# Performance work log

Measured on AMD Instinct MI355X. Metric: run time of the kernel, lower is better.

## Reference

```python
import jax, jax.numpy as jnp
import numpy as np

BS, NA = 32, 128
NE = NA * (NA - 1)            # fully-connected directed, no self loops
NU, D = 4, 8                  # num_user, per-user feature dim
FEAT = NU * D                 # 32: node / edge feature dim
CC = 8                        # conv1 out channels (1x1 conv, in_channels=2)
CONV_OUT = CC * NU * D        # 256
EMB = 64                      # embedding size (x_last / output dim)
H1 = 256                      # MLP hidden
MLP1_IN = CONV_OUT + EMB      # layer_idx > 1: concat local_state_j
MLP2_IN = FEAT + EMB + EMB    # x0, x_last, agg_in


def make_edges():
    src, dst = np.meshgrid(np.arange(NA), np.arange(NA), indexing='ij')
    m = src != dst
    return jnp.asarray(np.stack([src[m], dst[m]], axis=1), dtype=jnp.int32)


def setup_inputs() -> dict:
    key = jax.random.key(0)
    ks = jax.random.split(key, 9)
    return {
        "x0": jax.random.normal(ks[0], (BS, NA, FEAT), jnp.float32),
        "x_last": jax.random.normal(ks[1], (BS, NA, EMB), jnp.float32),
        "edge_attr": jax.random.normal(ks[2], (BS, NE, FEAT), jnp.float32),
        "conv_w": jax.random.normal(ks[3], (CC, 2), jnp.float32) * 0.3,
        "conv_b": jnp.zeros((CC,), jnp.float32),
        "mlp1_w1": jax.random.normal(ks[4], (MLP1_IN, H1), jnp.float32) * 0.05,
        "mlp1_b1": jnp.zeros((H1,), jnp.float32),
        "mlp1_w2": jax.random.normal(ks[5], (H1, EMB), jnp.float32) * 0.05,
        "mlp1_b2": jnp.zeros((EMB,), jnp.float32),
        "mlp2_w1": jax.random.normal(ks[6], (MLP2_IN, H1), jnp.float32) * 0.05,
        "mlp2_b1": jnp.zeros((H1,), jnp.float32),
        "mlp2_w2": jax.random.normal(ks[7], (H1, EMB), jnp.float32) * 0.05,
        "mlp2_b2": jnp.zeros((EMB,), jnp.float32),
        "edge_idx": make_edges(),
    }


def reference(x0, x_last, edge_attr, conv_w, conv_b,
              mlp1_w1, mlp1_b1, mlp1_w2, mlp1_b2,
              mlp2_w1, mlp2_b1, mlp2_w2, mlp2_b2, edge_idx):
    src, dst = edge_idx[:, 0], edge_idx[:, 1]
    # --- propagate / local_embedding ---
    nf_j = x0[:, src, :]                 # [B, E, FEAT] gather source node feats
    ls_j = x_last[:, src, :]             # [B, E, EMB]  (layer_idx > 1)
    # torch: cat(node_feat, edge_attr) on user dim then view [N,2,NU,D]
    x = jnp.stack([nf_j.reshape(BS, NE, NU, D),
                   edge_attr.reshape(BS, NE, NU, D)], axis=2)  # [B,E,2,NU,D]
    # 1x1 Conv2d(2 -> CC) + ReLU
    y = jax.nn.relu(jnp.einsum('becud,oc->beoud', x, conv_w)
                    + conv_b[None, None, :, None, None])
    y = y.reshape(BS, NE, CONV_OUT)
    lf = jnp.concatenate([y, ls_j], axis=-1)                   # [B,E,MLP1_IN]
    h = jax.nn.relu(lf @ mlp1_w1 + mlp1_b1)
    local_embed = h @ mlp1_w2 + mlp1_b2                        # [B,E,EMB]
    # per-node segment sum over destination (replaces python loop over agents)
    agg_in = jnp.zeros((BS, NA, EMB), local_embed.dtype).at[:, dst, :].add(local_embed)
    # --- update_embedding ---
    agg = jnp.concatenate([x0, x_last, agg_in], axis=-1)       # [B,NA,MLP2_IN]
    h2 = jax.nn.relu(agg @ mlp2_w1 + mlp2_b1)
    return h2 @ mlp2_w2 + mlp2_b2                              # [B,NA,EMB]
```

## Files before the change

### kernel.cpp

```cpp
#include <hip/hip_runtime.h>
#include <hip/hip_bf16.h>

#define BSg   32
#define NAg   128
#define NEg   16256
#define EMBg  64
#define H1g   256

typedef __attribute__((ext_vector_type(8))) short  short8;
typedef __attribute__((ext_vector_type(4))) float  f32x4;

__device__ __forceinline__ unsigned short f2bf16u(float x) {
    union { __hip_bfloat16 h; unsigned short u; } cv;
    cv.h = __float2bfloat16(x);
    return cv.u;
}
__device__ __forceinline__ unsigned int pack2(float a, float b) {
    union { __hip_bfloat162 h; unsigned int u; } cv;
    cv.h = __float22bfloat162_rn(make_float2(a, b));
    return cv.u;
}

__global__ void pack_weights(const float* __restrict__ w1, unsigned short* __restrict__ w1p)
{
    int i = blockIdx.x * 256 + threadIdx.x;
    if (i < 320 * 256) {
        int k = i >> 8, n = i & 255;
        w1p[(k >> 3) * (256 * 8) + n * 8 + (k & 7)] = f2bf16u(w1[i]);
    }
}

__global__ __launch_bounds__(512, 4) void edge_kernel(
    const float* __restrict__ x0, const float* __restrict__ x_last,
    const float* __restrict__ edge_attr, const float* __restrict__ conv_w,
    const float* __restrict__ conv_b, const unsigned short* __restrict__ w1p,
    const float* __restrict__ b1, const float* __restrict__ w2f,
    const float* __restrict__ b2, float* __restrict__ agg)
{
    __shared__ unsigned short fragA[2][10 * 4 * 64 * 8];

    const int tid  = threadIdx.x;
    const int b    = blockIdx.x >> 7;
    const int d    = blockIdx.x & 127;
    const int w8   = tid >> 6, lane = tid & 63;
    const int half = w8 >> 2, wq = w8 & 3;
    const int llo  = lane & 15, lhi = lane >> 4;
    const int colbase = wq * 64;

    short8 bf0[4];
    #pragma unroll
    for (int n = 0; n < 4; ++n)
        bf0[n] = *(const short8*)&w1p[(lhi * H1g + colbase + n * 16 + llo) * 8];

    {
        const int j  = wq * 16 + llo;
        const int el = half * 64 + j;
        int s = el + (el >= d ? 1 : 0);
        if (s > 127) s = 127;
        int e = s * 127 + d - (s < d ? 1 : 0);
        if (e > NEg - 1) e = NEg - 1;

        const float4* nfp = (const float4*)(x0        + (((size_t)b * NAg + s) << 5) + (lhi << 3));
        const float4* eap = (const float4*)(edge_attr + (((size_t)b * NEg + e) << 5) + (lhi << 3));
        float4 nf0 = nfp[0], nf1 = nfp[1];
        float4 ea0 = eap[0], ea1 = eap[1];

        #pragma unroll
        for (int o = 0; o < 8; ++o) {
            const float w0 = conv_w[2 * o], w1v = conv_w[2 * o + 1], cb = conv_b[o];
            float y0 = fmaxf(fmaf(w0, nf0.x, fmaf(w1v, ea0.x, cb)), 0.f);
            float y1 = fmaxf(fmaf(w0, nf0.y, fmaf(w1v, ea0.y, cb)), 0.f);
            float y2 = fmaxf(fmaf(w0, nf0.z, fmaf(w1v, ea0.z, cb)), 0.f);
            float y3 = fmaxf(fmaf(w0, nf0.w, fmaf(w1v, ea0.w, cb)), 0.f);
            float y4 = fmaxf(fmaf(w0, nf1.x, fmaf(w1v, ea1.x, cb)), 0.f);
            float y5 = fmaxf(fmaf(w0, nf1.y, fmaf(w1v, ea1.y, cb)), 0.f);
            float y6 = fmaxf(fmaf(w0, nf1.z, fmaf(w1v, ea1.z, cb)), 0.f);
            float y7 = fmaxf(fmaf(w0, nf1.w, fmaf(w1v, ea1.w, cb)), 0.f);
            uint4 pk;
            pk.x = pack2(y0, y1); pk.y = pack2(y2, y3);
            pk.z = pack2(y4, y5); pk.w = pack2(y6, y7);
            *(uint4*)&fragA[half][(((o * 4 + wq) * 64) + lane) * 8] = pk;
        }
        {
            const float4* lsp = (const float4*)(x_last + (((size_t)b * NAg + s) << 6) + (lhi << 4));
            float4 l0 = lsp[0], l1 = lsp[1], l2 = lsp[2], l3 = lsp[3];
            uint4 pa, pb;
            pa.x = pack2(l0.x, l0.y); pa.y = pack2(l0.z, l0.w);
            pa.z = pack2(l1.x, l1.y); pa.w = pack2(l1.z, l1.w);
            pb.x = pack2(l2.x, l2.y); pb.y = pack2(l2.z, l2.w);
            pb.z = pack2(l3.x, l3.y); pb.w = pack2(l3.z, l3.w);
            const int ks8  = 8 + (lhi >> 1);
            const int slot = (ks8 * 4 + wq) * 64 + ((lhi & 1) * 2) * 16 + llo;
            *(uint4*)&fragA[half][slot * 8]        = pa;
            *(uint4*)&fragA[half][(slot + 16) * 8] = pb;
        }
    }
    __syncthreads();

    f32x4 acc[4][4];
    #pragma unroll
    for (int m = 0; m < 4; ++m)
        #pragma unroll
        for (int n = 0; n < 4; ++n)
            acc[m][n] = (f32x4){0.f, 0.f, 0.f, 0.f};

    #pragma unroll
    for (int ks = 0; ks < 10; ++ks) {
        short8 af[4], bf[4];
        #pragma unroll
        for (int m = 0; m < 4; ++m)
            af[m] = *(const short8*)&fragA[half][((ks * 4 + m) * 64 + lane) * 8];
        #pragma unroll
        for (int n = 0; n < 4; ++n) {
            if (ks == 0) bf[n] = bf0[n];
            else         bf[n] = *(const short8*)&w1p[((ks * 4 + lhi) * H1g + colbase + n * 16 + llo) * 8];
        }
        #pragma unroll
        for (int m = 0; m < 4; ++m)
            #pragma unroll
            for (int n = 0; n < 4; ++n)
                acc[m][n] = __builtin_amdgcn_mfma_f32_16x16x32_bf16(af[m], bf[n], acc[m][n], 0, 0, 0);
    }

    float h1s[4];
    {
        float bias1[4];
        #pragma unroll
        for (int n = 0; n < 4; ++n) bias1[n] = b1[colbase + n * 16 + llo];
        #pragma unroll
        for (int n = 0; n < 4; ++n) {
            float p = 0.f;
            #pragma unroll
            for (int m = 0; m < 4; ++m)
                #pragma unroll
                for (int i = 0; i < 4; ++i) {
                    float v = fmaxf(acc[m][n][i] + bias1[n], 0.f);
                    if (!(m == 3 && i == 3) || !(half == 1 && lhi == 3)) p += v;
                }
            p += __shfl_xor(p, 16, 64);
            p += __shfl_xor(p, 32, 64);
            h1s[n] = p;
        }
    }
    __syncthreads();

    float* h1part = (float*)&fragA[0][0];
    float* redS   = h1part + 512;

    if (lhi == 0) {
        #pragma unroll
        for (int n = 0; n < 4; ++n) h1part[half * 256 + colbase + n * 16 + llo] = h1s[n];
    }
    __syncthreads();

    {
        const int c = tid & 63, kq = tid >> 6;
        float p = 0.f;
        #pragma unroll 8
        for (int k0 = 0; k0 < 32; ++k0) {
            int k = kq * 32 + k0;
            float h = h1part[k] + h1part[256 + k];
            p = fmaf(h, w2f[k * 64 + c], p);
        }
        redS[kq * 64 + c] = p;
    }
    __syncthreads();
    if (tid < 64) {
        float v = redS[tid]       + redS[64 + tid]  + redS[128 + tid] + redS[192 + tid]
                + redS[256 + tid] + redS[320 + tid] + redS[384 + tid] + redS[448 + tid]
                + 127.f * b2[tid];
        agg[(((size_t)b * NAg + d) << 6) + tid] = v;
    }
}

__global__ __launch_bounds__(256) void node_kernel(
    const float* __restrict__ x0, const float* __restrict__ x_last,
    const float* __restrict__ agg, const float* __restrict__ w1,
    const float* __restrict__ b1, const float* __restrict__ w2,
    const float* __restrict__ b2, float* __restrict__ out)
{
    __shared__ float lf[8][160];
    __shared__ float h2s[8][257];
    const int tid = threadIdx.x;
    const int r0  = blockIdx.x * 8;

    for (int idx = tid; idx < 8 * 160; idx += 256) {
        int r = idx / 160, c = idx % 160;
        int gr = r0 + r;
        int bb = gr >> 7, a = gr & 127;
        float v;
        if (c < 32)      v = x0[(((size_t)bb * NAg + a) << 5) + c];
        else if (c < 96) v = x_last[(((size_t)bb * NAg + a) << 6) + (c - 32)];
        else             v = agg[((size_t)gr << 6) + (c - 96)];
        lf[r][c] = v;
    }
    __syncthreads();

    {
        const int c = tid;
        float acc[8];
        const float bb = b1[c];
        #pragma unroll
        for (int r = 0; r < 8; ++r) acc[r] = bb;
        for (int k = 0; k < 160; ++k) {
            float wv = w1[k * 256 + c];
            #pragma unroll
            for (int r = 0; r < 8; ++r) acc[r] = fmaf(lf[r][k], wv, acc[r]);
        }
        #pragma unroll
        for (int r = 0; r < 8; ++r) h2s[r][c] = fmaxf(acc[r], 0.f);
    }
    __syncthreads();

    {
        const int n = tid & 63, rq = tid >> 6;
        float acc[2];
        const float bb = b2[n];
        #pragma unroll
        for (int j = 0; j < 2; ++j) acc[j] = bb;
        for (int k = 0; k < 256; ++k) {
            float wv = w2[k * 64 + n];
            #pragma unroll
            for (int j = 0; j < 2; ++j) acc[j] = fmaf(h2s[rq * 2 + j][k], wv, acc[j]);
        }
        #pragma unroll
        for (int j = 0; j < 2; ++j)
            out[((size_t)(r0 + rq * 2 + j) << 6) + n] = acc[j];
    }
}

extern "C" void kernel_launch(void* const* d_in, const int* in_sizes, int n_in,
                              void* d_out, int out_size, void* d_ws, size_t ws_size,
                              hipStream_t stream)
{
    const float* x0       = (const float*)d_in[0];
    const float* x_last   = (const float*)d_in[1];
    const float* edge_attr= (const float*)d_in[2];
    const float* conv_w   = (const float*)d_in[3];
    const float* conv_b   = (const float*)d_in[4];
    const float* mlp1_w1  = (const float*)d_in[5];
    const float* mlp1_b1  = (const float*)d_in[6];
    const float* mlp1_w2  = (const float*)d_in[7];
    const float* mlp1_b2  = (const float*)d_in[8];
    const float* mlp2_w1  = (const float*)d_in[9];
    const float* mlp2_b1  = (const float*)d_in[10];
    const float* mlp2_w2  = (const float*)d_in[11];
    const float* mlp2_b2  = (const float*)d_in[12];

    char* ws = (char*)d_ws;
    float* agg          = (float*)ws;
    unsigned short* w1p = (unsigned short*)(ws + (1 << 20));

    pack_weights<<<320, 256, 0, stream>>>(mlp1_w1, w1p);
    edge_kernel<<<BSg * NAg, 512, 0, stream>>>(x0, x_last, edge_attr, conv_w, conv_b,
                                               w1p, mlp1_b1, mlp1_w2, mlp1_b2, agg);
    node_kernel<<<(BSg * NAg) / 8, 256, 0, stream>>>(x0, x_last, agg, mlp2_w1, mlp2_b1,
                                                     mlp2_w2, mlp2_b2, (float*)d_out);
}
```

Measured before the change: 132.6 us.

## Split edge kernel into half-size blocks with atomic accumulation and XCD-aware remap

Each destination node's 128 source edges are now split across two 256-thread workgroups instead of one 512-thread block. Each half computes partial second-layer outputs and adds them into the aggregate buffer with atomicAdd, so the buffer is zeroed first with a memset. Block IDs are remapped so the two halves and neighbouring nodes land on the same XCD, with the intent of better L2 reuse. Smaller blocks and half the shared memory should raise occupancy and scheduling flexibility, at the cost of duplicated second-layer work, atomics and an extra memset.

```diff
diff --git a/kernel.cpp b/kernel.cpp
--- a/kernel.cpp
+++ b/kernel.cpp
@@ -30,20 +30,22 @@
     }
 }
 
-__global__ __launch_bounds__(512, 4) void edge_kernel(
+__global__ __launch_bounds__(256, 4) void edge_kernel(
     const float* __restrict__ x0, const float* __restrict__ x_last,
     const float* __restrict__ edge_attr, const float* __restrict__ conv_w,
     const float* __restrict__ conv_b, const unsigned short* __restrict__ w1p,
     const float* __restrict__ b1, const float* __restrict__ w2f,
     const float* __restrict__ b2, float* __restrict__ agg)
 {
-    __shared__ unsigned short fragA[2][10 * 4 * 64 * 8];
+    __shared__ unsigned short fragA[10 * 4 * 64 * 8];
+
+    const int wgid = (blockIdx.x & 7) * 1024 + (blockIdx.x >> 3);
+    const int half = wgid & 1;
+    const int bd   = wgid >> 1;
+    const int b    = bd >> 7, d = bd & 127;
 
     const int tid  = threadIdx.x;
-    const int b    = blockIdx.x >> 7;
-    const int d    = blockIdx.x & 127;
-    const int w8   = tid >> 6, lane = tid & 63;
-    const int half = w8 >> 2, wq = w8 & 3;
+    const int wq   = tid >> 6, lane = tid & 63;
     const int llo  = lane & 15, lhi = lane >> 4;
     const int colbase = wq * 64;
 
@@ -79,7 +81,7 @@
             uint4 pk;
             pk.x = pack2(y0, y1); pk.y = pack2(y2, y3);
             pk.z = pack2(y4, y5); pk.w = pack2(y6, y7);
-            *(uint4*)&fragA[half][(((o * 4 + wq) * 64) + lane) * 8] = pk;
+            *(uint4*)&fragA[(((o * 4 + wq) * 64) + lane) * 8] = pk;
         }
         {
             const float4* lsp = (const float4*)(x_last + (((size_t)b * NAg + s) << 6) + (lhi << 4));
@@ -91,8 +93,8 @@
             pb.z = pack2(l3.x, l3.y); pb.w = pack2(l3.z, l3.w);
             const int ks8  = 8 + (lhi >> 1);
             const int slot = (ks8 * 4 + wq) * 64 + ((lhi & 1) * 2) * 16 + llo;
-            *(uint4*)&fragA[half][slot * 8]        = pa;
-            *(uint4*)&fragA[half][(slot + 16) * 8] = pb;
+            *(uint4*)&fragA[slot * 8]        = pa;
+            *(uint4*)&fragA[(slot + 16) * 8] = pb;
         }
     }
     __syncthreads();
@@ -109,7 +111,7 @@
         short8 af[4], bf[4];
         #pragma unroll
         for (int m = 0; m < 4; ++m)
-            af[m] = *(const short8*)&fragA[half][((ks * 4 + m) * 64 + lane) * 8];
+            af[m] = *(const short8*)&fragA[((ks * 4 + m) * 64 + lane) * 8];
         #pragma unroll
         for (int n = 0; n < 4; ++n) {
             if (ks == 0) bf[n] = bf0[n];
@@ -135,7 +137,7 @@
                 #pragma unroll
                 for (int i = 0; i < 4; ++i) {
                     float v = fmaxf(acc[m][n][i] + bias1[n], 0.f);
-                    if (!(m == 3 && i == 3) || !(half == 1 && lhi == 3)) p += v;
+                    if (!(m == 3 && i == 3 && half == 1 && lhi == 3)) p += v;
                 }
             p += __shfl_xor(p, 16, 64);
             p += __shfl_xor(p, 32, 64);
@@ -144,12 +146,12 @@
     }
     __syncthreads();
 
-    float* h1part = (float*)&fragA[0][0];
-    float* redS   = h1part + 512;
+    float* h1part = (float*)fragA;
+    float* redS   = h1part + 256;
 
     if (lhi == 0) {
         #pragma unroll
-        for (int n = 0; n < 4; ++n) h1part[half * 256 + colbase + n * 16 + llo] = h1s[n];
+        for (int n = 0; n < 4; ++n) h1part[colbase + n * 16 + llo] = h1s[n];
     }
     __syncthreads();
 
@@ -157,19 +159,17 @@
         const int c = tid & 63, kq = tid >> 6;
         float p = 0.f;
         #pragma unroll 8
-        for (int k0 = 0; k0 < 32; ++k0) {
-            int k = kq * 32 + k0;
-            float h = h1part[k] + h1part[256 + k];
-            p = fmaf(h, w2f[k * 64 + c], p);
+        for (int k0 = 0; k0 < 64; ++k0) {
+            int k = kq * 64 + k0;
+            p = fmaf(h1part[k], w2f[k * 64 + c], p);
         }
         redS[kq * 64 + c] = p;
     }
     __syncthreads();
     if (tid < 64) {
-        float v = redS[tid]       + redS[64 + tid]  + redS[128 + tid] + redS[192 + tid]
-                + redS[256 + tid] + redS[320 + tid] + redS[384 + tid] + redS[448 + tid]
-                + 127.f * b2[tid];
-        agg[(((size_t)b * NAg + d) << 6) + tid] = v;
+        float v = redS[tid] + redS[64 + tid] + redS[128 + tid] + redS[192 + tid];
+        if (half == 0) v += 127.f * b2[tid];
+        atomicAdd(&agg[((size_t)bd << 6) + tid], v);
     }
 }
 
@@ -251,9 +251,10 @@
     float* agg          = (float*)ws;
     unsigned short* w1p = (unsigned short*)(ws + (1 << 20));
 
+    hipMemsetAsync(agg, 0, (size_t)BSg * NAg * EMBg * sizeof(float), stream);
     pack_weights<<<320, 256, 0, stream>>>(mlp1_w1, w1p);
-    edge_kernel<<<BSg * NAg, 512, 0, stream>>>(x0, x_last, edge_attr, conv_w, conv_b,
-                                               w1p, mlp1_b1, mlp1_w2, mlp1_b2, agg);
+    edge_kernel<<<BSg * NAg * 2, 256, 0, stream>>>(x0, x_last, edge_attr, conv_w, conv_b,
+                                                   w1p, mlp1_b1, mlp1_w2, mlp1_b2, agg);
     node_kernel<<<(BSg * NAg) / 8, 256, 0, stream>>>(x0, x_last, agg, mlp2_w1, mlp2_b1,
                                                      mlp2_w2, mlp2_b2, (float*)d_out);
 }
```

Measured after the change: 144.3 us. 1.09x slower.

## Repartition edge MLP so each wave owns its rows and drops a barrier

Applied to the files above, without the earlier changes.

Each wave of the edge kernel now computes its own 16 edge rows against all 256 hidden columns, rather than 64 rows by 64 columns. Since every wave reads only the A fragments it wrote itself, the barrier between staging and the MFMA loop goes away. Per-wave hidden partial sums now go straight into that wave's own LDS slice and are reduced across 8 partials in the second layer, which removes another barrier. The cost is that each wave streams all 256 packed weight columns from global memory, roughly four times more B-fragment loads per wave. Unroll pragmas are also added to the node kernel loops and the workspace buffers are reordered.

```diff
diff --git a/kernel.cpp b/kernel.cpp
--- a/kernel.cpp
+++ b/kernel.cpp
@@ -39,18 +39,14 @@
 {
     __shared__ unsigned short fragA[2][10 * 4 * 64 * 8];
 
+    const int bd = blockIdx.x;
+    const int b  = bd >> 7, d = bd & 127;
+
     const int tid  = threadIdx.x;
-    const int b    = blockIdx.x >> 7;
-    const int d    = blockIdx.x & 127;
     const int w8   = tid >> 6, lane = tid & 63;
     const int half = w8 >> 2, wq = w8 & 3;
     const int llo  = lane & 15, lhi = lane >> 4;
-    const int colbase = wq * 64;
-
-    short8 bf0[4];
-    #pragma unroll
-    for (int n = 0; n < 4; ++n)
-        bf0[n] = *(const short8*)&w1p[(lhi * H1g + colbase + n * 16 + llo) * 8];
+    const bool padthread = (half == 1 && wq == 3 && lhi == 3);
 
     {
         const int j  = wq * 16 + llo;
@@ -95,71 +91,52 @@
             *(uint4*)&fragA[half][(slot + 16) * 8] = pb;
         }
     }
-    __syncthreads();
-
-    f32x4 acc[4][4];
+
+    f32x4 acc[16];
     #pragma unroll
-    for (int m = 0; m < 4; ++m)
-        #pragma unroll
-        for (int n = 0; n < 4; ++n)
-            acc[m][n] = (f32x4){0.f, 0.f, 0.f, 0.f};
+    for (int n = 0; n < 16; ++n)
+        acc[n] = (f32x4){0.f, 0.f, 0.f, 0.f};
 
     #pragma unroll
     for (int ks = 0; ks < 10; ++ks) {
-        short8 af[4], bf[4];
-        #pragma unroll
-        for (int m = 0; m < 4; ++m)
-            af[m] = *(const short8*)&fragA[half][((ks * 4 + m) * 64 + lane) * 8];
-        #pragma unroll
-        for (int n = 0; n < 4; ++n) {
-            if (ks == 0) bf[n] = bf0[n];
-            else         bf[n] = *(const short8*)&w1p[((ks * 4 + lhi) * H1g + colbase + n * 16 + llo) * 8];
-        }
-        #pragma unroll
-        for (int m = 0; m < 4; ++m)
-            #pragma unroll
-            for (int n = 0; n < 4; ++n)
-                acc[m][n] = __builtin_amdgcn_mfma_f32_16x16x32_bf16(af[m], bf[n], acc[m][n], 0, 0, 0);
-    }
-
-    float h1s[4];
-    {
-        float bias1[4];
-        #pragma unroll
-        for (int n = 0; n < 4; ++n) bias1[n] = b1[colbase + n * 16 + llo];
-        #pragma unroll
-        for (int n = 0; n < 4; ++n) {
+        short8 af = *(const short8*)&fragA[half][((ks * 4 + wq) * 64 + lane) * 8];
+        #pragma unroll
+        for (int n = 0; n < 16; ++n) {
+            short8 bf = *(const short8*)&w1p[((ks * 4 + lhi) * H1g + n * 16 + llo) * 8];
+            acc[n] = __builtin_amdgcn_mfma_f32_16x16x32_bf16(af, bf, acc[n], 0, 0, 0);
+        }
+    }
+
+    {
+        float* myh1 = (float*)&fragA[half][(wq * 64) * 8];
+        #pragma unroll
+        for (int n = 0; n < 16; ++n) {
+            const float bias = b1[n * 16 + llo];
             float p = 0.f;
             #pragma unroll
-            for (int m = 0; m < 4; ++m)
-                #pragma unroll
-                for (int i = 0; i < 4; ++i) {
-                    float v = fmaxf(acc[m][n][i] + bias1[n], 0.f);
-                    if (!(m == 3 && i == 3) || !(half == 1 && lhi == 3)) p += v;
-                }
+            for (int i = 0; i < 4; ++i) {
+                float v = fmaxf(acc[n][i] + bias, 0.f);
+                if (!(padthread && i == 3)) p += v;
+            }
             p += __shfl_xor(p, 16, 64);
             p += __shfl_xor(p, 32, 64);
-            h1s[n] = p;
-        }
-    }
-    __syncthreads();
-
-    float* h1part = (float*)&fragA[0][0];
-    float* redS   = h1part + 512;
-
-    if (lhi == 0) {
-        #pragma unroll
-        for (int n = 0; n < 4; ++n) h1part[half * 256 + colbase + n * 16 + llo] = h1s[n];
-    }
-    __syncthreads();
-
-    {
-        const int c = tid & 63, kq = tid >> 6;
+            if (lhi == 0) myh1[n * 16 + llo] = p;
+        }
+    }
+    __syncthreads();
+
+    const float* F0 = (const float*)&fragA[0][0];
+    const float* F1 = (const float*)&fragA[1][0];
+    float* redS = (float*)&fragA[0][0] + 1024;
+
+    {
+        const int c = tid & 63, kq = w8;
         float p = 0.f;
-        #pragma unroll 8
+        #pragma unroll 4
         for (int k0 = 0; k0 < 32; ++k0) {
             int k = kq * 32 + k0;
-            float h = h1part[k] + h1part[256 + k];
+            float h = F0[k] + F0[256 + k] + F0[512 + k] + F0[768 + k]
+                    + F1[k] + F1[256 + k] + F1[512 + k] + F1[768 + k];
             p = fmaf(h, w2f[k * 64 + c], p);
         }
         redS[kq * 64 + c] = p;
@@ -169,7 +146,7 @@
         float v = redS[tid]       + redS[64 + tid]  + redS[128 + tid] + redS[192 + tid]
                 + redS[256 + tid] + redS[320 + tid] + redS[384 + tid] + redS[448 + tid]
                 + 127.f * b2[tid];
-        agg[(((size_t)b * NAg + d) << 6) + tid] = v;
+        agg[((size_t)bd << 6) + tid] = v;
     }
 }
 
@@ -202,6 +179,7 @@
         const float bb = b1[c];
         #pragma unroll
         for (int r = 0; r < 8; ++r) acc[r] = bb;
+        #pragma unroll 4
         for (int k = 0; k < 160; ++k) {
             float wv = w1[k * 256 + c];
             #pragma unroll
@@ -218,6 +196,7 @@
         const float bb = b2[n];
         #pragma unroll
         for (int j = 0; j < 2; ++j) acc[j] = bb;
+        #pragma unroll 4
         for (int k = 0; k < 256; ++k) {
             float wv = w2[k * 64 + n];
             #pragma unroll
@@ -248,8 +227,8 @@
     const float* mlp2_b2  = (const float*)d_in[12];
 
     char* ws = (char*)d_ws;
-    float* agg          = (float*)ws;
-    unsigned short* w1p = (unsigned short*)(ws + (1 << 20));
+    unsigned short* w1p = (unsigned short*)ws;
+    float* agg          = (float*)(ws + (1 << 20));
 
     pack_weights<<<320, 256, 0, stream>>>(mlp1_w1, w1p);
     edge_kernel<<<BSg * NAg, 512, 0, stream>>>(x0, x_last, edge_attr, conv_w, conv_b,
```

Measured after the change: 233.5 us. 1.76x slower.
